# Kernel tuning notes

Hardware: AMD Instinct MI355X
Metric: run time of the kernel (lower is better)

Reference implementation:

```python
import jax, jax.numpy as jnp
import numpy as np

BETA = 0.95
SG_SLOPE = 25.0

@jax.custom_vjp
def spike(mem, thr):
    return (mem > thr).astype(mem.dtype)

def _spike_fwd(mem, thr):
    return spike(mem, thr), (mem, thr)

def _spike_bwd(res, g):
    mem, thr = res
    s = jax.nn.sigmoid(SG_SLOPE * (mem - thr))
    return (g * (SG_SLOPE * s * (1.0 - s)), jnp.zeros_like(thr))

spike.defvjp(_spike_fwd, _spike_bwd)

def setup_inputs() -> dict:
    key = jax.random.key(0)
    ks = jax.random.split(key, 7)
    T, B, IN, H, OUT = 50, 512, 784, 800, 10
    return {
        "x":  jax.random.normal(ks[0], (T, B, IN), dtype=jnp.float32),
        "W1": jax.random.normal(ks[1], (H, IN), dtype=jnp.float32) / np.sqrt(IN),
        "b1": jax.random.normal(ks[2], (H,), dtype=jnp.float32) * 0.01,
        "W2": jax.random.normal(ks[3], (H, H), dtype=jnp.float32) / np.sqrt(H),
        "b2": jax.random.normal(ks[4], (H,), dtype=jnp.float32) * 0.01,
        "W3": jax.random.normal(ks[5], (OUT, H), dtype=jnp.float32) / np.sqrt(H),
        "b3": jax.random.normal(ks[6], (OUT,), dtype=jnp.float32) * 0.01,
        "thresh1": jnp.ones((H,), dtype=jnp.float32),
        "thresh2": jnp.ones((H,), dtype=jnp.float32),
    }

def reference(x, W1, b1, W2, b2, W3, b3, thresh1, thresh2):
    T, B = x.shape[0], x.shape[1]
    H, OUT = W1.shape[0], W3.shape[0]
    # Batch the input projection across all timesteps: [T,B,H]
    x1 = jnp.einsum('tbi,hi->tbh', x, W1) + b1

    def step(carry, xt):
        mem1, mem2, mem3 = carry
        mem1 = BETA * mem1 + xt
        spk1 = spike(mem1, thresh1)
        mem1 = mem1 * (1.0 - spk1)
        mem2 = BETA * mem2 + spk1 @ W2.T + b2
        spk2 = spike(mem2, thresh2)
        mem2 = mem2 * (1.0 - spk2)
        mem3 = BETA * mem3 + spk2 @ W3.T + b3
        spk3 = spike(mem3, jnp.float32(1.0))
        mem3 = mem3 * (1.0 - spk3)
        return (mem1, mem2, mem3), (spk1, spk2, spk3)

    init = (jnp.zeros((B, H), x.dtype), jnp.zeros((B, H), x.dtype), jnp.zeros((B, OUT), x.dtype))
    _, (s1r, s2r, s3r) = jax.lax.scan(step, init, x1)
    return s3r.sum(0), s1r, s2r, s3r
```

## Files before the change

### kernel.cpp

```cpp
#include <hip/hip_runtime.h>

#define TT 50
#define BB 512
#define II 784
#define HH 800
#define OO 10
#define BH (BB*HH)
#define MM (TT*BB)

__global__ __launch_bounds__(256) void k_gemm1(
    const float* __restrict__ x, const float* __restrict__ W1,
    const float* __restrict__ b1, double* __restrict__ x1d)
{
    __shared__ double As[16*130];
    __shared__ double Bs[16*82];
    const int m0 = blockIdx.x * 128;
    const int n0 = blockIdx.y * 80;
    const int tid = threadIdx.x;
    const int tx = tid & 15, ty = tid >> 4;
    double acc[8][5] = {};

    const int sm = tid >> 1;
    const int sk = (tid & 1) * 8;
    const int bq0n = tid >> 2, bq0k = (tid & 3) * 4;
    const int q1 = tid + 256;
    const int bq1n = q1 >> 2, bq1k = (q1 & 3) * 4;

    for (int k0 = 0; k0 < II; k0 += 16) {
        const float4 a0 = *(const float4*)(x + (long)(m0+sm)*II + k0 + sk);
        const float4 a1 = *(const float4*)(x + (long)(m0+sm)*II + k0 + sk + 4);
        const float4 bv0 = *(const float4*)(W1 + (long)(n0+bq0n)*II + k0 + bq0k);
        float4 bv1;
        if (tid < 64)
            bv1 = *(const float4*)(W1 + (long)(n0+bq1n)*II + k0 + bq1k);
        __syncthreads();
        As[(sk+0)*130+sm] = (double)a0.x;
        As[(sk+1)*130+sm] = (double)a0.y;
        As[(sk+2)*130+sm] = (double)a0.z;
        As[(sk+3)*130+sm] = (double)a0.w;
        As[(sk+4)*130+sm] = (double)a1.x;
        As[(sk+5)*130+sm] = (double)a1.y;
        As[(sk+6)*130+sm] = (double)a1.z;
        As[(sk+7)*130+sm] = (double)a1.w;
        Bs[(bq0k+0)*82+bq0n] = (double)bv0.x;
        Bs[(bq0k+1)*82+bq0n] = (double)bv0.y;
        Bs[(bq0k+2)*82+bq0n] = (double)bv0.z;
        Bs[(bq0k+3)*82+bq0n] = (double)bv0.w;
        if (tid < 64) {
            Bs[(bq1k+0)*82+bq1n] = (double)bv1.x;
            Bs[(bq1k+1)*82+bq1n] = (double)bv1.y;
            Bs[(bq1k+2)*82+bq1n] = (double)bv1.z;
            Bs[(bq1k+3)*82+bq1n] = (double)bv1.w;
        }
        __syncthreads();
        #pragma unroll
        for (int k = 0; k < 16; ++k) {
            double a[8], b[5];
            #pragma unroll
            for (int i = 0; i < 8; ++i) a[i] = As[k*130 + ty + 16*i];
            #pragma unroll
            for (int j = 0; j < 5; ++j) b[j] = Bs[k*82 + tx + 16*j];
            #pragma unroll
            for (int i = 0; i < 8; ++i)
                #pragma unroll
                for (int j = 0; j < 5; ++j)
                    acc[i][j] = fma(a[i], b[j], acc[i][j]);
        }
    }
    #pragma unroll
    for (int i = 0; i < 8; ++i) {
        const long m = m0 + ty + 16*i;
        #pragma unroll
        for (int j = 0; j < 5; ++j) {
            const int n = n0 + tx + 16*j;
            x1d[m*HH + n] = acc[i][j] + (double)b1[n];
        }
    }
}

__global__ __launch_bounds__(256) void k_mem1(
    const double* __restrict__ x1d, const float* __restrict__ thresh1,
    unsigned char* __restrict__ s1c, float* __restrict__ s1r)
{
    const int lid = blockIdx.x*256 + threadIdx.x;
    const int h = lid % HH;
    const double th = (double)thresh1[h];
    double mem = 0.0;
    for (int t = 0; t < TT; ++t) {
        const long idx = (long)t*BH + lid;
        mem = 0.95*mem + x1d[idx];
        const bool spk = mem > th;
        s1c[idx] = spk ? 1 : 0;
        s1r[idx] = spk ? 1.0f : 0.0f;
        if (spk) mem = 0.0;
    }
}

__global__ __launch_bounds__(256) void k_gemm2(
    const unsigned char* __restrict__ s1c, const float* __restrict__ W2,
    float* __restrict__ z2)
{
    __shared__ float As[32*132];
    __shared__ float Bs[32*84];
    const int m0 = blockIdx.x * 128;
    const int n0 = blockIdx.y * 80;
    const int tid = threadIdx.x;
    const int tx = tid & 15, ty = tid >> 4;
    float acc[8][5] = {};

    const int sm = tid >> 1;
    const int sk = (tid & 1) * 16;
    const int b0n = tid >> 3,        b0k = (tid & 7) * 4;
    const int q1 = tid + 256, b1n = q1 >> 3, b1k = (q1 & 7) * 4;
    const int q2 = tid + 512, b2n = q2 >> 3, b2k = (q2 & 7) * 4;

    for (int k0 = 0; k0 < HH; k0 += 32) {
        const uint4 av = *(const uint4*)(s1c + (long)(m0+sm)*HH + k0 + sk);
        const float4 w0 = *(const float4*)(W2 + (long)(n0+b0n)*HH + k0 + b0k);
        const float4 w1 = *(const float4*)(W2 + (long)(n0+b1n)*HH + k0 + b1k);
        float4 w2;
        if (tid < 128)
            w2 = *(const float4*)(W2 + (long)(n0+b2n)*HH + k0 + b2k);
        __syncthreads();
        {
            const unsigned int d[4] = {av.x, av.y, av.z, av.w};
            #pragma unroll
            for (int w = 0; w < 4; ++w) {
                #pragma unroll
                for (int j = 0; j < 4; ++j)
                    As[(sk + w*4 + j)*132 + sm] =
                        (float)((d[w] >> (8*j)) & 0xffu);
            }
        }
        Bs[(b0k+0)*84+b0n] = w0.x; Bs[(b0k+1)*84+b0n] = w0.y;
        Bs[(b0k+2)*84+b0n] = w0.z; Bs[(b0k+3)*84+b0n] = w0.w;
        Bs[(b1k+0)*84+b1n] = w1.x; Bs[(b1k+1)*84+b1n] = w1.y;
        Bs[(b1k+2)*84+b1n] = w1.z; Bs[(b1k+3)*84+b1n] = w1.w;
        if (tid < 128) {
            Bs[(b2k+0)*84+b2n] = w2.x; Bs[(b2k+1)*84+b2n] = w2.y;
            Bs[(b2k+2)*84+b2n] = w2.z; Bs[(b2k+3)*84+b2n] = w2.w;
        }
        __syncthreads();
        #pragma unroll
        for (int k = 0; k < 32; ++k) {
            float a[8], b[5];
            #pragma unroll
            for (int i = 0; i < 8; ++i) a[i] = As[k*132 + ty*8 + i];
            #pragma unroll
            for (int j = 0; j < 4; ++j) b[j] = Bs[k*84 + tx*4 + j];
            b[4] = Bs[k*84 + 64 + tx];
            #pragma unroll
            for (int i = 0; i < 8; ++i)
                #pragma unroll
                for (int j = 0; j < 5; ++j)
                    acc[i][j] = __fmaf_rn(a[i], b[j], acc[i][j]);
        }
    }
    #pragma unroll
    for (int i = 0; i < 8; ++i) {
        const long m = m0 + ty*8 + i;
        #pragma unroll
        for (int j = 0; j < 4; ++j)
            z2[m*HH + n0 + tx*4 + j] = acc[i][j];
        z2[m*HH + n0 + 64 + tx] = acc[i][4];
    }
}

__global__ __launch_bounds__(256) void k_scan2(
    const float* __restrict__ z2, const float* __restrict__ b2,
    const float* __restrict__ thresh2, float* __restrict__ s2r,
    unsigned char* __restrict__ s2c)
{
    const int lid = blockIdx.x*256 + threadIdx.x;
    const int n = lid % HH;
    const float b2v = b2[n];
    const float thv = thresh2[n];
    float m = 0.0f;
    for (int t = 0; t < TT; ++t) {
        const long idx = (long)t*BH + lid;
        const float m2 = __fadd_rn(
            __fadd_rn(__fmul_rn(0.95f, m), z2[idx]), b2v);
        const bool spk = m2 > thv;
        s2r[idx] = spk ? 1.0f : 0.0f;
        s2c[idx] = spk ? 1 : 0;
        m = spk ? 0.0f : m2;
    }
}

__global__ __launch_bounds__(256) void k_gemm3(
    const unsigned char* __restrict__ s2c, const float* __restrict__ W3,
    float* __restrict__ z3)
{
    const long m = blockIdx.x*256 + threadIdx.x;
    const unsigned char* row = s2c + m*HH;
    float acc[10] = {};
    for (int k0 = 0; k0 < HH; k0 += 16) {
        const uint4 v = *(const uint4*)(row + k0);
        const unsigned int d[4] = {v.x, v.y, v.z, v.w};
        #pragma unroll
        for (int w = 0; w < 4; ++w) {
            #pragma unroll
            for (int j = 0; j < 4; ++j) {
                const float sv = (float)((d[w] >> (8*j)) & 0xffu);
                const int k = k0 + w*4 + j;
                #pragma unroll
                for (int o = 0; o < 10; ++o)
                    acc[o] = __fmaf_rn(sv, W3[o*HH + k], acc[o]);
            }
        }
    }
    #pragma unroll
    for (int o = 0; o < 10; ++o)
        z3[m*OO + o] = acc[o];
}

__global__ __launch_bounds__(256) void k_scan3(
    const float* __restrict__ z3, const float* __restrict__ b3,
    float* __restrict__ s3r, float* __restrict__ out0)
{
    const int gid = blockIdx.x*256 + threadIdx.x;
    if (gid >= BB*OO) return;
    const int o = gid % OO;
    const float b3v = b3[o];
    float mem = 0.0f, cnt = 0.0f;
    for (int t = 0; t < TT; ++t) {
        const float m3 = __fadd_rn(
            __fadd_rn(__fmul_rn(0.95f, mem), z3[(long)t*BB*OO + gid]), b3v);
        const bool spk = m3 > 1.0f;
        s3r[(long)t*BB*OO + gid] = spk ? 1.0f : 0.0f;
        if (spk) cnt = __fadd_rn(cnt, 1.0f);
        mem = spk ? 0.0f : m3;
    }
    out0[gid] = cnt;
}

extern "C" void kernel_launch(void* const* d_in, const int* in_sizes, int n_in,
                              void* d_out, int out_size, void* d_ws, size_t ws_size,
                              hipStream_t stream)
{
    const float* x   = (const float*)d_in[0];
    const float* W1  = (const float*)d_in[1];
    const float* b1  = (const float*)d_in[2];
    const float* W2  = (const float*)d_in[3];
    const float* b2  = (const float*)d_in[4];
    const float* W3  = (const float*)d_in[5];
    const float* b3  = (const float*)d_in[6];
    const float* th1 = (const float*)d_in[7];
    const float* th2 = (const float*)d_in[8];

    float* out0 = (float*)d_out;
    float* s1r  = out0 + BB*OO;
    float* s2r  = s1r + (long)TT*BH;
    float* s3r  = s2r + (long)TT*BH;

    char* p = (char*)d_ws;
    double* x1d = (double*)p;
    float*  z2  = (float*)p;
    float*  z3  = (float*)(p + 84000000);
    unsigned char* s1c = (unsigned char*)(p + 163840000);
    unsigned char* s2c = s1c + (size_t)TT*BH;
    (void)ws_size;

    k_gemm1<<<dim3(200,10), dim3(256), 0, stream>>>(x, W1, b1, x1d);
    k_mem1 <<<dim3(1600),   dim3(256), 0, stream>>>(x1d, th1, s1c, s1r);
    k_gemm2<<<dim3(200,10), dim3(256), 0, stream>>>(s1c, W2, z2);
    k_scan2<<<dim3(1600),   dim3(256), 0, stream>>>(z2, b2, th2, s2r, s2c);
    k_gemm3<<<dim3(100),    dim3(256), 0, stream>>>(s2c, W3, z3);
    k_scan3<<<dim3(20),     dim3(256), 0, stream>>>(z3, b3, s3r, out0);
}
```

Measured before the change: 1.481 ms.

## Double-buffer shared memory in both GEMM kernels and swap grid order

Both tiled GEMMs now use two shared-memory buffers with smaller K-chunks. The next tile is loaded into registers while the current one is computed, so each iteration needs only one barrier. The grid is transposed so the N blocks vary fastest, which lets blocks that share an A row panel run together for L2 reuse. LDS reads become vectorized (double2/float4) through a contiguous ty*8 row mapping, and gemm2 writes its output with float4 stores. The smaller K-chunks mean more loop iterations and barriers, and the changed A-row mapping may add LDS bank conflicts in the double-precision kernel.

```diff
diff --git a/kernel.cpp b/kernel.cpp
--- a/kernel.cpp
+++ b/kernel.cpp
@@ -12,70 +12,75 @@
     const float* __restrict__ x, const float* __restrict__ W1,
     const float* __restrict__ b1, double* __restrict__ x1d)
 {
-    __shared__ double As[16*130];
-    __shared__ double Bs[16*82];
-    const int m0 = blockIdx.x * 128;
-    const int n0 = blockIdx.y * 80;
+    __shared__ double As[2][8*130];
+    __shared__ double Bs[2][8*82];
+    const int n0 = blockIdx.x * 80;
+    const int m0 = blockIdx.y * 128;
     const int tid = threadIdx.x;
     const int tx = tid & 15, ty = tid >> 4;
     double acc[8][5] = {};
 
-    const int sm = tid >> 1;
-    const int sk = (tid & 1) * 8;
-    const int bq0n = tid >> 2, bq0k = (tid & 3) * 4;
-    const int q1 = tid + 256;
-    const int bq1n = q1 >> 2, bq1k = (q1 & 3) * 4;
-
-    for (int k0 = 0; k0 < II; k0 += 16) {
-        const float4 a0 = *(const float4*)(x + (long)(m0+sm)*II + k0 + sk);
-        const float4 a1 = *(const float4*)(x + (long)(m0+sm)*II + k0 + sk + 4);
-        const float4 bv0 = *(const float4*)(W1 + (long)(n0+bq0n)*II + k0 + bq0k);
-        float4 bv1;
-        if (tid < 64)
-            bv1 = *(const float4*)(W1 + (long)(n0+bq1n)*II + k0 + bq1k);
-        __syncthreads();
-        As[(sk+0)*130+sm] = (double)a0.x;
-        As[(sk+1)*130+sm] = (double)a0.y;
-        As[(sk+2)*130+sm] = (double)a0.z;
-        As[(sk+3)*130+sm] = (double)a0.w;
-        As[(sk+4)*130+sm] = (double)a1.x;
-        As[(sk+5)*130+sm] = (double)a1.y;
-        As[(sk+6)*130+sm] = (double)a1.z;
-        As[(sk+7)*130+sm] = (double)a1.w;
-        Bs[(bq0k+0)*82+bq0n] = (double)bv0.x;
-        Bs[(bq0k+1)*82+bq0n] = (double)bv0.y;
-        Bs[(bq0k+2)*82+bq0n] = (double)bv0.z;
-        Bs[(bq0k+3)*82+bq0n] = (double)bv0.w;
-        if (tid < 64) {
-            Bs[(bq1k+0)*82+bq1n] = (double)bv1.x;
-            Bs[(bq1k+1)*82+bq1n] = (double)bv1.y;
-            Bs[(bq1k+2)*82+bq1n] = (double)bv1.z;
-            Bs[(bq1k+3)*82+bq1n] = (double)bv1.w;
-        }
-        __syncthreads();
-        #pragma unroll
-        for (int k = 0; k < 16; ++k) {
-            double a[8], b[5];
-            #pragma unroll
-            for (int i = 0; i < 8; ++i) a[i] = As[k*130 + ty + 16*i];
-            #pragma unroll
-            for (int j = 0; j < 5; ++j) b[j] = Bs[k*82 + tx + 16*j];
+    const int ar = tid >> 1;
+    const int ak = (tid & 1) * 4;
+    const float* aptr = x + (long)(m0 + ar) * II + ak;
+    const int br = tid >> 1;
+    const int bk = (tid & 1) * 4;
+    const float* bptr = W1 + (long)(n0 + br) * II + bk;
+    const bool bact = tid < 160;
+
+    float4 afr = *(const float4*)(aptr);
+    float4 bfr = bact ? *(const float4*)(bptr) : make_float4(0.f,0.f,0.f,0.f);
+
+#define STAGE1(BUF) do {                                                    \
+        As[BUF][(ak+0)*130+ar] = (double)afr.x;                             \
+        As[BUF][(ak+1)*130+ar] = (double)afr.y;                             \
+        As[BUF][(ak+2)*130+ar] = (double)afr.z;                             \
+        As[BUF][(ak+3)*130+ar] = (double)afr.w;                             \
+        if (bact) {                                                         \
+            Bs[BUF][(bk+0)*82+br] = (double)bfr.x;                          \
+            Bs[BUF][(bk+1)*82+br] = (double)bfr.y;                          \
+            Bs[BUF][(bk+2)*82+br] = (double)bfr.z;                          \
+            Bs[BUF][(bk+3)*82+br] = (double)bfr.w;                          \
+        }                                                                   \
+    } while (0)
+
+    STAGE1(0);
+    __syncthreads();
+    for (int c = 0; c < 98; ++c) {
+        const int cur = c & 1;
+        if (c < 97) {
+            afr = *(const float4*)(aptr + (c+1)*8);
+            if (bact) bfr = *(const float4*)(bptr + (c+1)*8);
+        }
+        #pragma unroll
+        for (int k = 0; k < 8; ++k) {
+            const double2* Ap = (const double2*)&As[cur][k*130 + ty*8];
+            const double2 a01 = Ap[0], a23 = Ap[1], a45 = Ap[2], a67 = Ap[3];
+            double bv[5];
+            #pragma unroll
+            for (int j = 0; j < 5; ++j) bv[j] = Bs[cur][k*82 + tx + 16*j];
+            const double am[8] = {a01.x, a01.y, a23.x, a23.y,
+                                  a45.x, a45.y, a67.x, a67.y};
             #pragma unroll
             for (int i = 0; i < 8; ++i)
                 #pragma unroll
                 for (int j = 0; j < 5; ++j)
-                    acc[i][j] = fma(a[i], b[j], acc[i][j]);
-        }
-    }
+                    acc[i][j] = fma(am[i], bv[j], acc[i][j]);
+        }
+        if (c < 97) STAGE1(cur ^ 1);
+        __syncthreads();
+    }
+    double bb[5];
+    #pragma unroll
+    for (int j = 0; j < 5; ++j) bb[j] = (double)b1[n0 + tx + 16*j];
     #pragma unroll
     for (int i = 0; i < 8; ++i) {
-        const long m = m0 + ty + 16*i;
-        #pragma unroll
-        for (int j = 0; j < 5; ++j) {
-            const int n = n0 + tx + 16*j;
-            x1d[m*HH + n] = acc[i][j] + (double)b1[n];
-        }
-    }
+        const long m = m0 + ty*8 + i;
+        #pragma unroll
+        for (int j = 0; j < 5; ++j)
+            x1d[m*HH + n0 + tx + 16*j] = acc[i][j] + bb[j];
+    }
+#undef STAGE1
 }
 
 __global__ __launch_bounds__(256) void k_mem1(
@@ -100,70 +105,84 @@
     const unsigned char* __restrict__ s1c, const float* __restrict__ W2,
     float* __restrict__ z2)
 {
-    __shared__ float As[32*132];
-    __shared__ float Bs[32*84];
-    const int m0 = blockIdx.x * 128;
-    const int n0 = blockIdx.y * 80;
+    __shared__ float As[2][16*132];
+    __shared__ float Bs[2][16*84];
+    const int n0 = blockIdx.x * 80;
+    const int m0 = blockIdx.y * 128;
     const int tid = threadIdx.x;
     const int tx = tid & 15, ty = tid >> 4;
     float acc[8][5] = {};
 
-    const int sm = tid >> 1;
-    const int sk = (tid & 1) * 16;
-    const int b0n = tid >> 3,        b0k = (tid & 7) * 4;
-    const int q1 = tid + 256, b1n = q1 >> 3, b1k = (q1 & 7) * 4;
-    const int q2 = tid + 512, b2n = q2 >> 3, b2k = (q2 & 7) * 4;
-
-    for (int k0 = 0; k0 < HH; k0 += 32) {
-        const uint4 av = *(const uint4*)(s1c + (long)(m0+sm)*HH + k0 + sk);
-        const float4 w0 = *(const float4*)(W2 + (long)(n0+b0n)*HH + k0 + b0k);
-        const float4 w1 = *(const float4*)(W2 + (long)(n0+b1n)*HH + k0 + b1k);
-        float4 w2;
-        if (tid < 128)
-            w2 = *(const float4*)(W2 + (long)(n0+b2n)*HH + k0 + b2k);
-        __syncthreads();
-        {
-            const unsigned int d[4] = {av.x, av.y, av.z, av.w};
-            #pragma unroll
-            for (int w = 0; w < 4; ++w) {
-                #pragma unroll
-                for (int j = 0; j < 4; ++j)
-                    As[(sk + w*4 + j)*132 + sm] =
-                        (float)((d[w] >> (8*j)) & 0xffu);
-            }
-        }
-        Bs[(b0k+0)*84+b0n] = w0.x; Bs[(b0k+1)*84+b0n] = w0.y;
-        Bs[(b0k+2)*84+b0n] = w0.z; Bs[(b0k+3)*84+b0n] = w0.w;
-        Bs[(b1k+0)*84+b1n] = w1.x; Bs[(b1k+1)*84+b1n] = w1.y;
-        Bs[(b1k+2)*84+b1n] = w1.z; Bs[(b1k+3)*84+b1n] = w1.w;
-        if (tid < 128) {
-            Bs[(b2k+0)*84+b2n] = w2.x; Bs[(b2k+1)*84+b2n] = w2.y;
-            Bs[(b2k+2)*84+b2n] = w2.z; Bs[(b2k+3)*84+b2n] = w2.w;
-        }
-        __syncthreads();
-        #pragma unroll
-        for (int k = 0; k < 32; ++k) {
-            float a[8], b[5];
-            #pragma unroll
-            for (int i = 0; i < 8; ++i) a[i] = As[k*132 + ty*8 + i];
-            #pragma unroll
-            for (int j = 0; j < 4; ++j) b[j] = Bs[k*84 + tx*4 + j];
-            b[4] = Bs[k*84 + 64 + tx];
+    const int ar = tid >> 1;
+    const int ak = (tid & 1) * 8;
+    const unsigned char* aptr = s1c + (long)(m0 + ar)*HH + ak;
+    const int b0r = tid >> 2,        b0k = (tid & 3) * 4;
+    const int q1 = tid + 256;
+    const int b1r = q1 >> 2,         b1k = (q1 & 3) * 4;
+    const float* bptr0 = W2 + (long)(n0 + b0r)*HH + b0k;
+    const float* bptr1 = W2 + (long)(n0 + b1r)*HH + b1k;
+    const bool bact = tid < 64;
+
+    uint2 au = *(const uint2*)(aptr);
+    float4 bf0 = *(const float4*)(bptr0);
+    float4 bf1 = bact ? *(const float4*)(bptr1) : make_float4(0.f,0.f,0.f,0.f);
+
+#define STAGE2(BUF) do {                                                    \
+        const unsigned int d0 = au.x, d1 = au.y;                            \
+        As[BUF][(ak+0)*132+ar] = (float)( d0        & 0xffu);               \
+        As[BUF][(ak+1)*132+ar] = (float)((d0 >>  8) & 0xffu);               \
+        As[BUF][(ak+2)*132+ar] = (float)((d0 >> 16) & 0xffu);               \
+        As[BUF][(ak+3)*132+ar] = (float)((d0 >> 24) & 0xffu);               \
+        As[BUF][(ak+4)*132+ar] = (float)( d1        & 0xffu);               \
+        As[BUF][(ak+5)*132+ar] = (float)((d1 >>  8) & 0xffu);               \
+        As[BUF][(ak+6)*132+ar] = (float)((d1 >> 16) & 0xffu);               \
+        As[BUF][(ak+7)*132+ar] = (float)((d1 >> 24) & 0xffu);               \
+        Bs[BUF][(b0k+0)*84+b0r] = bf0.x;                                    \
+        Bs[BUF][(b0k+1)*84+b0r] = bf0.y;                                    \
+        Bs[BUF][(b0k+2)*84+b0r] = bf0.z;                                    \
+        Bs[BUF][(b0k+3)*84+b0r] = bf0.w;                                    \
+        if (bact) {                                                         \
+            Bs[BUF][(b1k+0)*84+b1r] = bf1.x;                                \
+            Bs[BUF][(b1k+1)*84+b1r] = bf1.y;                                \
+            Bs[BUF][(b1k+2)*84+b1r] = bf1.z;                                \
+            Bs[BUF][(b1k+3)*84+b1r] = bf1.w;                                \
+        }                                                                   \
+    } while (0)
+
+    STAGE2(0);
+    __syncthreads();
+    for (int c = 0; c < 50; ++c) {
+        const int cur = c & 1;
+        if (c < 49) {
+            au = *(const uint2*)(aptr + (c+1)*16);
+            bf0 = *(const float4*)(bptr0 + (c+1)*16);
+            if (bact) bf1 = *(const float4*)(bptr1 + (c+1)*16);
+        }
+        #pragma unroll
+        for (int k = 0; k < 16; ++k) {
+            const float4 A0 = *(const float4*)&As[cur][k*132 + ty*8];
+            const float4 A1 = *(const float4*)&As[cur][k*132 + ty*8 + 4];
+            const float4 Bv = *(const float4*)&Bs[cur][k*84 + tx*4];
+            const float  b4 = Bs[cur][k*84 + 64 + tx];
+            const float am[8] = {A0.x, A0.y, A0.z, A0.w, A1.x, A1.y, A1.z, A1.w};
+            const float bv[5] = {Bv.x, Bv.y, Bv.z, Bv.w, b4};
             #pragma unroll
             for (int i = 0; i < 8; ++i)
                 #pragma unroll
                 for (int j = 0; j < 5; ++j)
-                    acc[i][j] = __fmaf_rn(a[i], b[j], acc[i][j]);
-        }
+                    acc[i][j] = __fmaf_rn(am[i], bv[j], acc[i][j]);
+        }
+        if (c < 49) STAGE2(cur ^ 1);
+        __syncthreads();
     }
     #pragma unroll
     for (int i = 0; i < 8; ++i) {
         const long m = m0 + ty*8 + i;
-        #pragma unroll
-        for (int j = 0; j < 4; ++j)
-            z2[m*HH + n0 + tx*4 + j] = acc[i][j];
+        *(float4*)&z2[m*HH + n0 + tx*4] =
+            make_float4(acc[i][0], acc[i][1], acc[i][2], acc[i][3]);
         z2[m*HH + n0 + 64 + tx] = acc[i][4];
     }
+#undef STAGE2
 }
 
 __global__ __launch_bounds__(256) void k_scan2(
@@ -261,9 +280,9 @@
     unsigned char* s2c = s1c + (size_t)TT*BH;
     (void)ws_size;
 
-    k_gemm1<<<dim3(200,10), dim3(256), 0, stream>>>(x, W1, b1, x1d);
+    k_gemm1<<<dim3(10,200), dim3(256), 0, stream>>>(x, W1, b1, x1d);
     k_mem1 <<<dim3(1600),   dim3(256), 0, stream>>>(x1d, th1, s1c, s1r);
-    k_gemm2<<<dim3(200,10), dim3(256), 0, stream>>>(s1c, W2, z2);
+    k_gemm2<<<dim3(10,200), dim3(256), 0, stream>>>(s1c, W2, z2);
     k_scan2<<<dim3(1600),   dim3(256), 0, stream>>>(z2, b2, th2, s2r, s2c);
     k_gemm3<<<dim3(100),    dim3(256), 0, stream>>>(s2c, W3, z3);
     k_scan3<<<dim3(20),     dim3(256), 0, stream>>>(z3, b3, s3r, out0);
```

Result: slower. 2.100 ms (+41.7%).
